# Kernel tuning notes

Measured on AMD Instinct MI355X. Metric: run time of the kernel, lower is better.

The kernel has to match this reference:

```python
import jax, jax.numpy as jnp
import numpy as np

B, C, W, R = 8, 512, 2048, 8
CR = C // R


def setup_inputs() -> dict:
    key = jax.random.key(0)
    ks = jax.random.split(key, 7)
    s = 0.02
    return {
        "x": jax.random.normal(ks[0], (B, C, W), dtype=jnp.float32),
        "wq": jax.random.normal(ks[1], (CR, C), dtype=jnp.float32) * s,
        "bq": jnp.zeros((CR,), dtype=jnp.float32),
        "wk": jax.random.normal(ks[2], (CR, C), dtype=jnp.float32) * s,
        "bk": jnp.zeros((CR,), dtype=jnp.float32),
        "wv": jax.random.normal(ks[3], (C, C), dtype=jnp.float32) * s,
        "bv": jnp.zeros((C,), dtype=jnp.float32),
    }


def reference(x, wq, bq, wk, bk, wv, bv):
    # conv1x1 == per-position linear over channel dim
    q = jnp.einsum("oc,bcw->bow", wq, x) + bq[:, None]   # [B, C//R, W]
    k = jnp.einsum("oc,bcw->bow", wk, x) + bk[:, None]   # [B, C//R, W]
    v = jnp.einsum("oc,bcw->bow", wv, x) + bv[:, None]   # [B, C, W]
    scale = q.shape[1] ** -0.5
    # scores[b, i, j] = sum_d q[b, d, i] * k[b, d, j]
    scores = jnp.einsum("bdi,bdj->bij", q, k) * scale     # [B, W, W]
    attn = jax.nn.softmax(scores, axis=-1)
    # context[b, c, j] = sum_i v[b, c, i] * attn[b, i, j]  (bmm(value, attn))
    context = jnp.einsum("bci,bij->bcj", v, attn)         # [B, C, W]
    return context + x
```

## Files before the change

kernel.cpp:

```cpp
#include <hip/hip_runtime.h>
#include <hip/hip_bf16.h>


#define B 8
#define C 512
#define W 2048
#define CR 64
static constexpr float SCALE = 0.125f;

typedef __bf16 bf16x8 __attribute__((ext_vector_type(8)));
typedef float f32x4 __attribute__((ext_vector_type(4)));
typedef unsigned char uchar;
typedef unsigned long long ull;

__device__ inline ushort f2bs(float f) {
    __hip_bfloat16 h = __float2bfloat16(f);
    return *reinterpret_cast<ushort*>(&h);
}
__device__ inline f32x4 mfma16(bf16x8 a, bf16x8 b, f32x4 c) {
    return __builtin_amdgcn_mfma_f32_16x16x32_bf16(a, b, c, 0, 0, 0);
}
__device__ inline f32x4 mfma8(long long a, long long b, f32x4 c) {
    return __builtin_amdgcn_mfma_f32_16x16x32_fp8_fp8(a, b, c, 0, 0, 0);
}

__device__ inline uchar f2fp8(float f) {
#if __has_builtin(__builtin_amdgcn_cvt_pk_fp8_f32)
    int v = __builtin_amdgcn_cvt_pk_fp8_f32(f, f, 0, false);
    return (uchar)(v & 0xFF);
#else
    unsigned u = __float_as_uint(f);
    uchar s = (uchar)((u >> 24) & 0x80);
    float a = fabsf(f);
    if (a >= 448.0f) return s | 0x7E;
    if (a < 0.015625f) {
        int m = (int)rintf(a * 512.0f);
        if (m > 7) return s | 0x08;
        return s | (uchar)m;
    }
    int e; float m = frexpf(a, &e);
    int Eb = e - 1 + 7;
    int mant = (int)rintf((m * 2.0f - 1.0f) * 8.0f);
    if (mant == 8) { mant = 0; Eb++; }
    if (Eb > 15 || (Eb == 15 && mant > 6)) return s | 0x7E;
    return s | (uchar)(Eb << 3) | (uchar)mant;
#endif
}

__device__ inline size_t vpf8_idx(int b, int c, int i) {
    return (((size_t)(b * 32 + (i >> 6)) * 32 + (c >> 4)) << 10)
         + (((i >> 5) & 1) << 9) + ((((c & 15) | (((i >> 3) & 3) << 4))) << 3) + (i & 7);
}


__global__ __launch_bounds__(256) void cast_w(
    const float* __restrict__ wq, const float* __restrict__ wk, const float* __restrict__ wv,
    ushort* __restrict__ wqb, ushort* __restrict__ wkb, ushort* __restrict__ wvb)
{
    int i = blockIdx.x * 256 + threadIdx.x;
    if (i < CR * C) { wqb[i] = f2bs(wq[i]); wkb[i] = f2bs(wk[i]); }
    if (i < C * C)  { wvb[i] = f2bs(wv[i]); }
}

__global__ __launch_bounds__(256) void castT_kernel(
    const float* __restrict__ x, ushort* __restrict__ xb)
{
    __shared__ __align__(16) ushort tile[64][72];
    const int b = blockIdx.z, c0 = blockIdx.y * 64, w0 = blockIdx.x * 64;
    const int t = threadIdx.x;
    for (int idx = t; idx < 64 * 64; idx += 256) {
        int c = idx >> 6, w = idx & 63;
        tile[w][c] = f2bs(x[(b * C + c0 + c) * W + w0 + w]);
    }
    __syncthreads();
    for (int idx = t; idx < 64 * 8; idx += 256) {
        int w = idx >> 3, u = idx & 7;
        *(bf16x8*)&xb[((size_t)b * W + w0 + w) * C + c0 + u * 8] = *(const bf16x8*)&tile[w][u * 8];
    }
}

__global__ __launch_bounds__(128) void proj_qk2_kernel(
    const ushort* __restrict__ xb, const ushort* __restrict__ wqb, const ushort* __restrict__ wkb,
    const float* __restrict__ bqf, const float* __restrict__ bkf,
    ushort* __restrict__ qT, ushort* __restrict__ kT)
{
    const int bid = blockIdx.x;
    const int b = bid & 7;
    const int w0 = (bid >> 3) * 64 + (threadIdx.x >> 6) * 32;
    const int lane = threadIdx.x & 63;
    const int lr = lane & 15, lg = lane >> 4;

    f32x4 accq[2][4] = {};
    f32x4 acck[2][4] = {};
    for (int kk = 0; kk < 16; ++kk) {
        const int ko = kk * 32 + (lg << 3);
        bf16x8 a[2], fq[4], fk[4];
        #pragma unroll
        for (int mf = 0; mf < 2; ++mf)
            a[mf] = *(const bf16x8*)&xb[((size_t)b * W + w0 + mf * 16 + lr) * C + ko];
        #pragma unroll
        for (int nf = 0; nf < 4; ++nf) {
            fq[nf] = *(const bf16x8*)&wqb[(nf * 16 + lr) * C + ko];
            fk[nf] = *(const bf16x8*)&wkb[(nf * 16 + lr) * C + ko];
        }
        #pragma unroll
        for (int mf = 0; mf < 2; ++mf)
            #pragma unroll
            for (int nf = 0; nf < 4; ++nf) {
                accq[mf][nf] = mfma16(a[mf], fq[nf], accq[mf][nf]);
                acck[mf][nf] = mfma16(a[mf], fk[nf], acck[mf][nf]);
            }
    }
    #pragma unroll
    for (int nf = 0; nf < 4; ++nf) {
        const int d = nf * 16 + lr;
        const float bqv = bqf[d], bkv = bkf[d];
        #pragma unroll
        for (int mf = 0; mf < 2; ++mf)
            #pragma unroll
            for (int r = 0; r < 4; ++r) {
                int w = w0 + mf * 16 + (lg << 2) + r;
                qT[(b * W + w) * CR + d] = f2bs(accq[mf][nf][r] + bqv);
                kT[(b * W + w) * CR + d] = f2bs(acck[mf][nf][r] + bkv);
            }
    }
}

__global__ __launch_bounds__(512) void qk_expf8_kernel(
    const ushort* __restrict__ qT, const ushort* __restrict__ kT,
    uchar* __restrict__ PuF8, float* __restrict__ ilrow)
{
    __shared__ __align__(8) uchar ptb[8][64][72];
    __shared__ float red[8][64];
    const int bid = blockIdx.x;
    const int b = bid & 7;
    const int i0 = (bid >> 3) * 64;
    const int it = i0 >> 6;
    const int t = threadIdx.x;
    const int w = t >> 6, lane = t & 63;
    const int lr = lane & 15, lg = lane >> 4;

    bf16x8 bq[4][2];
    #pragma unroll
    for (int nf = 0; nf < 4; ++nf)
        #pragma unroll
        for (int kk = 0; kk < 2; ++kk)
            bq[nf][kk] = *(const bf16x8*)&qT[(b * W + i0 + nf * 16 + lr) * CR + kk * 32 + (lg << 3)];

    float lacc[4] = {0.f, 0.f, 0.f, 0.f};
    for (int jt = 0; jt < 4; ++jt) {
        const int j0 = (jt * 8 + w) * 64;
        #pragma unroll
        for (int mf = 0; mf < 4; ++mf) {
            bf16x8 akf[2];
            #pragma unroll
            for (int kk = 0; kk < 2; ++kk)
                akf[kk] = *(const bf16x8*)&kT[(b * W + j0 + mf * 16 + lr) * CR + kk * 32 + (lg << 3)];
            f32x4 s[4] = {};
            #pragma unroll
            for (int kk = 0; kk < 2; ++kk)
                #pragma unroll
                for (int nf = 0; nf < 4; ++nf)
                    s[nf] = mfma16(akf[kk], bq[nf][kk], s[nf]);
            #pragma unroll
            for (int nf = 0; nf < 4; ++nf)
                #pragma unroll
                for (int r = 0; r < 4; ++r) {
                    float e = __expf(s[nf][r] * SCALE);
                    lacc[nf] += e;
                    ptb[w][mf * 16 + (lg << 2) + r][nf * 16 + lr] = f2fp8(e);
                }
        }
        #pragma unroll
        for (int mf = 0; mf < 4; ++mf) {
            const int jl = mf * 16 + (lane & 15);
            const size_t tbase = (((size_t)(b * 32 + it) * 128 + (j0 >> 4) + mf) << 10);
            #pragma unroll
            for (int kk = 0; kk < 2; ++kk) {
                const int ikb = (kk << 5) | ((lane >> 4) << 3);
                ull val = *(const ull*)&ptb[w][jl][ikb];
                *(ull*)&PuF8[tbase + (kk << 9) + ((size_t)lane << 3)] = val;
            }
        }
    }
    #pragma unroll
    for (int nf = 0; nf < 4; ++nf) {
        lacc[nf] += __shfl_xor(lacc[nf], 16);
        lacc[nf] += __shfl_xor(lacc[nf], 32);
        if (lg == 0) red[w][nf * 16 + lr] = lacc[nf];
    }
    __syncthreads();
    if (t < 64) {
        float ll = 0.f;
        #pragma unroll
        for (int g = 0; g < 8; ++g) ll += red[g][t];
        ilrow[b * W + i0 + t] = 1.0f / ll;
    }
}

__global__ __launch_bounds__(512) void proj_v2f8_kernel(
    const ushort* __restrict__ xb, const ushort* __restrict__ wvb, const float* __restrict__ bvf,
    const float* __restrict__ ilw, uchar* __restrict__ vpF8)
{
    const int bid = blockIdx.x;
    const int b = bid & 7;
    const int ct = (bid >> 3) & 3;
    const int wt = bid >> 5;
    const int wid = threadIdx.x >> 6, lane = threadIdx.x & 63;
    const int c0 = ct * 128 + (wid >> 2) * 64;
    const int w0 = wt * 256 + (wid & 3) * 64;
    const int lr = lane & 15, lg = lane >> 4;

    f32x4 acc[4][4] = {};
    for (int kk = 0; kk < 16; ++kk) {
        const int ko = kk * 32 + (lg << 3);
        bf16x8 a[4], bb[4];
        #pragma unroll
        for (int mf = 0; mf < 4; ++mf)
            a[mf] = *(const bf16x8*)&wvb[(c0 + mf * 16 + lr) * C + ko];
        #pragma unroll
        for (int nf = 0; nf < 4; ++nf)
            bb[nf] = *(const bf16x8*)&xb[((size_t)b * W + w0 + nf * 16 + lr) * C + ko];
        #pragma unroll
        for (int mf = 0; mf < 4; ++mf)
            #pragma unroll
            for (int nf = 0; nf < 4; ++nf)
                acc[mf][nf] = mfma16(a[mf], bb[nf], acc[mf][nf]);
    }
    float ilv[4];
    #pragma unroll
    for (int nf = 0; nf < 4; ++nf)
        ilv[nf] = ilw[b * W + w0 + nf * 16 + lr] * 1024.0f;
    #pragma unroll
    for (int mf = 0; mf < 4; ++mf) {
        #pragma unroll
        for (int r = 0; r < 4; ++r) {
            const int c = c0 + mf * 16 + (lg << 2) + r;
            const float bvv = bvf[c];
            #pragma unroll
            for (int nf = 0; nf < 4; ++nf) {
                int w = w0 + nf * 16 + lr;
                vpF8[vpf8_idx(b, c, w)] = f2fp8((acc[mf][nf][r] + bvv) * ilv[nf]);
            }
        }
    }
}

__global__ __launch_bounds__(512, 2) void pv38_kernel(
    const float* __restrict__ x, const uchar* __restrict__ vpF8, const uchar* __restrict__ PuF8,
    float* __restrict__ out)
{
    const int bid = blockIdx.x;
    const int b = bid & 7;
    const int j0 = (bid >> 3) * 64;
    const int w = threadIdx.x >> 6, lane = threadIdx.x & 63;
    const int lr = lane & 15, lg = lane >> 4;
    const int c0 = w * 64;
    const int ct0 = c0 >> 4;
    const int jt0 = j0 >> 4;
    const int NIT = W / 64;
    const int lo = lane * 8;

    long long a_cur[4][2], a_nxt[4][2], b_cur[4][2], b_nxt[4][2];
    #pragma unroll
    for (int mf = 0; mf < 4; ++mf)
        #pragma unroll
        for (int kk = 0; kk < 2; ++kk)
            a_cur[mf][kk] = *(const long long*)&vpF8[(((size_t)(b * 32 + 0) * 32 + ct0 + mf) << 10) + (kk << 9) + lo];
    #pragma unroll
    for (int nf = 0; nf < 4; ++nf)
        #pragma unroll
        for (int kk = 0; kk < 2; ++kk)
            b_cur[nf][kk] = *(const long long*)&PuF8[(((size_t)(b * 32 + 0) * 128 + jt0 + nf) << 10) + (kk << 9) + lo];

    f32x4 acc[4][4] = {};
    for (int it = 0; it < NIT; ++it) {
        const int in = (it + 1 < NIT) ? (it + 1) : it;
        #pragma unroll
        for (int mf = 0; mf < 4; ++mf)
            #pragma unroll
            for (int kk = 0; kk < 2; ++kk)
                a_nxt[mf][kk] = *(const long long*)&vpF8[(((size_t)(b * 32 + in) * 32 + ct0 + mf) << 10) + (kk << 9) + lo];
        #pragma unroll
        for (int nf = 0; nf < 4; ++nf)
            #pragma unroll
            for (int kk = 0; kk < 2; ++kk)
                b_nxt[nf][kk] = *(const long long*)&PuF8[(((size_t)(b * 32 + in) * 128 + jt0 + nf) << 10) + (kk << 9) + lo];
        #pragma unroll
        for (int kk = 0; kk < 2; ++kk)
            #pragma unroll
            for (int mf = 0; mf < 4; ++mf)
                #pragma unroll
                for (int nf = 0; nf < 4; ++nf)
                    acc[mf][nf] = mfma8(a_cur[mf][kk], b_cur[nf][kk], acc[mf][nf]);
        #pragma unroll
        for (int mf = 0; mf < 4; ++mf)
            #pragma unroll
            for (int kk = 0; kk < 2; ++kk)
                a_cur[mf][kk] = a_nxt[mf][kk];
        #pragma unroll
        for (int nf = 0; nf < 4; ++nf)
            #pragma unroll
            for (int kk = 0; kk < 2; ++kk)
                b_cur[nf][kk] = b_nxt[nf][kk];
    }
    #pragma unroll
    for (int mf = 0; mf < 4; ++mf)
        #pragma unroll
        for (int nf = 0; nf < 4; ++nf)
            #pragma unroll
            for (int r = 0; r < 4; ++r) {
                int c = c0 + mf * 16 + (lg << 2) + r;
                int j = j0 + nf * 16 + lr;
                int off = (b * C + c) * W + j;
                out[off] = acc[mf][nf][r] * 0.0009765625f + x[off];
            }
}

extern "C" void kernel_launch(void* const* d_in, const int* in_sizes, int n_in,
                              void* d_out, int out_size, void* d_ws, size_t ws_size,
                              hipStream_t stream) {
    const float* x  = (const float*)d_in[0];
    const float* wq = (const float*)d_in[1];
    const float* bq = (const float*)d_in[2];
    const float* wk = (const float*)d_in[3];
    const float* bk = (const float*)d_in[4];
    const float* wv = (const float*)d_in[5];
    const float* bv = (const float*)d_in[6];
    float* out = (float*)d_out;

    char* ws = (char*)d_ws;
    ushort* qTw  = (ushort*)(ws);
    ushort* kTw  = (ushort*)(ws + (2u << 20));
    uchar*  vpF8 = (uchar*)(ws + (4u << 20));
    ushort* xbw  = (ushort*)(ws + (20u << 20));
    ushort* wqb  = (ushort*)(ws + (36u << 20));
    ushort* wkb  = (ushort*)(ws + (36u << 20) + (64u << 10));
    ushort* wvb  = (ushort*)(ws + (36u << 20) + (128u << 10));
    float*  ilrw = (float*)(ws + (36u << 20) + (640u << 10));
    uchar*  PuF8 = (uchar*)(ws + (37u << 20));

    cast_w<<<dim3(1024), 256, 0, stream>>>(wq, wk, wv, wqb, wkb, wvb);
    castT_kernel<<<dim3(W / 64, C / 64, B), 256, 0, stream>>>(x, xbw);
    proj_qk2_kernel<<<dim3(W / 64 * B), 128, 0, stream>>>(xbw, wqb, wkb, bq, bk, qTw, kTw);
    qk_expf8_kernel<<<dim3(W / 64 * B), 512, 0, stream>>>(qTw, kTw, PuF8, ilrw);
    proj_v2f8_kernel<<<dim3(W / 256 * (C / 128) * B), 512, 0, stream>>>(xbw, wvb, bv, ilrw, vpF8);
    pv38_kernel<<<dim3(W / 64 * B), 512, 0, stream>>>(x, vpF8, PuF8, out);
}
```

Before: 127.3 us.

## Split PV kernel K-loop across two wave groups with shared-memory reduction

The PV fp8 GEMM kernel now launches 1024 threads per block. Two halves of 8 waves each process half of the reduction dimension, 16 iterations instead of 32. Their partial accumulators are combined through a shared-memory buffer before the residual add and store. This shortens each wave's serial MFMA/load chain and doubles the waves in flight to hide latency. The cost is extra syncthreads, 32KB of LDS, and possibly fewer resident blocks per CU.

```diff
diff --git a/kernel.cpp b/kernel.cpp
--- a/kernel.cpp
+++ b/kernel.cpp
@@ -246,19 +246,24 @@
     }
 }
 
-__global__ __launch_bounds__(512, 2) void pv38_kernel(
+__global__ __launch_bounds__(1024) void pv38_kernel(
     const float* __restrict__ x, const uchar* __restrict__ vpF8, const uchar* __restrict__ PuF8,
     float* __restrict__ out)
 {
+    __shared__ float redacc[8][64][16];
     const int bid = blockIdx.x;
     const int b = bid & 7;
     const int j0 = (bid >> 3) * 64;
-    const int w = threadIdx.x >> 6, lane = threadIdx.x & 63;
+    const int t = threadIdx.x;
+    const int w16 = t >> 6, lane = t & 63;
+    const int cs = w16 & 7;
+    const int half = w16 >> 3;
     const int lr = lane & 15, lg = lane >> 4;
-    const int c0 = w * 64;
+    const int c0 = cs * 64;
     const int ct0 = c0 >> 4;
     const int jt0 = j0 >> 4;
-    const int NIT = W / 64;
+    const int NIT = 16;
+    const int itb = half * 16;
     const int lo = lane * 8;
 
     long long a_cur[4][2], a_nxt[4][2], b_cur[4][2], b_nxt[4][2];
@@ -266,16 +271,16 @@
     for (int mf = 0; mf < 4; ++mf)
         #pragma unroll
         for (int kk = 0; kk < 2; ++kk)
-            a_cur[mf][kk] = *(const long long*)&vpF8[(((size_t)(b * 32 + 0) * 32 + ct0 + mf) << 10) + (kk << 9) + lo];
+            a_cur[mf][kk] = *(const long long*)&vpF8[(((size_t)(b * 32 + itb) * 32 + ct0 + mf) << 10) + (kk << 9) + lo];
     #pragma unroll
     for (int nf = 0; nf < 4; ++nf)
         #pragma unroll
         for (int kk = 0; kk < 2; ++kk)
-            b_cur[nf][kk] = *(const long long*)&PuF8[(((size_t)(b * 32 + 0) * 128 + jt0 + nf) << 10) + (kk << 9) + lo];
+            b_cur[nf][kk] = *(const long long*)&PuF8[(((size_t)(b * 32 + itb) * 128 + jt0 + nf) << 10) + (kk << 9) + lo];
 
     f32x4 acc[4][4] = {};
     for (int it = 0; it < NIT; ++it) {
-        const int in = (it + 1 < NIT) ? (it + 1) : it;
+        const int in = itb + ((it + 1 < NIT) ? (it + 1) : it);
         #pragma unroll
         for (int mf = 0; mf < 4; ++mf)
             #pragma unroll
@@ -305,16 +310,29 @@
                 b_cur[nf][kk] = b_nxt[nf][kk];
     }
     #pragma unroll
-    for (int mf = 0; mf < 4; ++mf)
-        #pragma unroll
-        for (int nf = 0; nf < 4; ++nf)
-            #pragma unroll
-            for (int r = 0; r < 4; ++r) {
-                int c = c0 + mf * 16 + (lg << 2) + r;
-                int j = j0 + nf * 16 + lr;
-                int off = (b * C + c) * W + j;
-                out[off] = acc[mf][nf][r] * 0.0009765625f + x[off];
-            }
+    for (int mf = 0; mf < 4; ++mf) {
+        __syncthreads();
+        if (half == 1) {
+            #pragma unroll
+            for (int nf = 0; nf < 4; ++nf)
+                #pragma unroll
+                for (int r = 0; r < 4; ++r)
+                    redacc[cs][lane][nf * 4 + r] = acc[mf][nf][r];
+        }
+        __syncthreads();
+        if (half == 0) {
+            #pragma unroll
+            for (int nf = 0; nf < 4; ++nf)
+                #pragma unroll
+                for (int r = 0; r < 4; ++r) {
+                    float sum = acc[mf][nf][r] + redacc[cs][lane][nf * 4 + r];
+                    int c = c0 + mf * 16 + (lg << 2) + r;
+                    int j = j0 + nf * 16 + lr;
+                    int off = (b * C + c) * W + j;
+                    out[off] = sum * 0.0009765625f + x[off];
+                }
+        }
+    }
 }
 
 extern "C" void kernel_launch(void* const* d_in, const int* in_sizes, int n_in,
@@ -345,5 +363,5 @@
     proj_qk2_kernel<<<dim3(W / 64 * B), 128, 0, stream>>>(xbw, wqb, wkb, bq, bk, qTw, kTw);
     qk_expf8_kernel<<<dim3(W / 64 * B), 512, 0, stream>>>(qTw, kTw, PuF8, ilrw);
     proj_v2f8_kernel<<<dim3(W / 256 * (C / 128) * B), 512, 0, stream>>>(xbw, wvb, bv, ilrw, vpF8);
-    pv38_kernel<<<dim3(W / 64 * B), 512, 0, stream>>>(x, vpF8, PuF8, out);
-}
+    pv38_kernel<<<dim3(W / 64 * B), 1024, 0, stream>>>(x, vpF8, PuF8, out);
+}
```

Result: no change. 128.7 us (+1.1%).

## Deepen PV prefetch to two stages and vectorize transpose-cast with larger tiles

Applied to the files above, without the earlier changes.

The PV fp8 MFMA loop now keeps two iterations of A/B fragments in flight instead of one, so global load latency has more time to be hidden behind the MFMAs. The launch-bounds occupancy hint of 2 blocks per CU is dropped so the extra registers fit. The x transpose-cast kernel now uses 128x128 tiles with float4 global loads instead of scalar loads. The risks are lower occupancy in PV from the added registers, and more LDS bank conflicts from the scalar column writes into the padded tile.

```diff
diff --git a/kernel.cpp b/kernel.cpp
--- a/kernel.cpp
+++ b/kernel.cpp
@@ -65,16 +65,21 @@
 __global__ __launch_bounds__(256) void castT_kernel(
     const float* __restrict__ x, ushort* __restrict__ xb)
 {
-    __shared__ __align__(16) ushort tile[64][72];
-    const int b = blockIdx.z, c0 = blockIdx.y * 64, w0 = blockIdx.x * 64;
+    __shared__ __align__(16) ushort tile[128][136];
+    const int b = blockIdx.z, c0 = blockIdx.y * 128, w0 = blockIdx.x * 128;
     const int t = threadIdx.x;
-    for (int idx = t; idx < 64 * 64; idx += 256) {
-        int c = idx >> 6, w = idx & 63;
-        tile[w][c] = f2bs(x[(b * C + c0 + c) * W + w0 + w]);
+    for (int idx = t; idx < 128 * 32; idx += 256) {
+        int c = idx >> 5, u = idx & 31;
+        f32x4 v4 = *(const f32x4*)&x[((size_t)b * C + c0 + c) * W + w0 + u * 4];
+        int w = u * 4;
+        tile[w + 0][c] = f2bs(v4[0]);
+        tile[w + 1][c] = f2bs(v4[1]);
+        tile[w + 2][c] = f2bs(v4[2]);
+        tile[w + 3][c] = f2bs(v4[3]);
     }
     __syncthreads();
-    for (int idx = t; idx < 64 * 8; idx += 256) {
-        int w = idx >> 3, u = idx & 7;
+    for (int idx = t; idx < 128 * 16; idx += 256) {
+        int w = idx >> 4, u = idx & 15;
         *(bf16x8*)&xb[((size_t)b * W + w0 + w) * C + c0 + u * 8] = *(const bf16x8*)&tile[w][u * 8];
     }
 }
@@ -246,7 +251,7 @@
     }
 }
 
-__global__ __launch_bounds__(512, 2) void pv38_kernel(
+__global__ __launch_bounds__(512) void pv38_kernel(
     const float* __restrict__ x, const uchar* __restrict__ vpF8, const uchar* __restrict__ PuF8,
     float* __restrict__ out)
 {
@@ -261,31 +266,36 @@
     const int NIT = W / 64;
     const int lo = lane * 8;
 
-    long long a_cur[4][2], a_nxt[4][2], b_cur[4][2], b_nxt[4][2];
+    long long a_cur[4][2], a_n1[4][2], a_n2[4][2];
+    long long b_cur[4][2], b_n1[4][2], b_n2[4][2];
     #pragma unroll
     for (int mf = 0; mf < 4; ++mf)
         #pragma unroll
-        for (int kk = 0; kk < 2; ++kk)
+        for (int kk = 0; kk < 2; ++kk) {
             a_cur[mf][kk] = *(const long long*)&vpF8[(((size_t)(b * 32 + 0) * 32 + ct0 + mf) << 10) + (kk << 9) + lo];
+            a_n1[mf][kk]  = *(const long long*)&vpF8[(((size_t)(b * 32 + 1) * 32 + ct0 + mf) << 10) + (kk << 9) + lo];
+        }
     #pragma unroll
     for (int nf = 0; nf < 4; ++nf)
         #pragma unroll
-        for (int kk = 0; kk < 2; ++kk)
+        for (int kk = 0; kk < 2; ++kk) {
             b_cur[nf][kk] = *(const long long*)&PuF8[(((size_t)(b * 32 + 0) * 128 + jt0 + nf) << 10) + (kk << 9) + lo];
+            b_n1[nf][kk]  = *(const long long*)&PuF8[(((size_t)(b * 32 + 1) * 128 + jt0 + nf) << 10) + (kk << 9) + lo];
+        }
 
     f32x4 acc[4][4] = {};
     for (int it = 0; it < NIT; ++it) {
-        const int in = (it + 1 < NIT) ? (it + 1) : it;
+        const int in = (it + 2 < NIT) ? (it + 2) : (NIT - 1);
         #pragma unroll
         for (int mf = 0; mf < 4; ++mf)
             #pragma unroll
             for (int kk = 0; kk < 2; ++kk)
-                a_nxt[mf][kk] = *(const long long*)&vpF8[(((size_t)(b * 32 + in) * 32 + ct0 + mf) << 10) + (kk << 9) + lo];
+                a_n2[mf][kk] = *(const long long*)&vpF8[(((size_t)(b * 32 + in) * 32 + ct0 + mf) << 10) + (kk << 9) + lo];
         #pragma unroll
         for (int nf = 0; nf < 4; ++nf)
             #pragma unroll
             for (int kk = 0; kk < 2; ++kk)
-                b_nxt[nf][kk] = *(const long long*)&PuF8[(((size_t)(b * 32 + in) * 128 + jt0 + nf) << 10) + (kk << 9) + lo];
+                b_n2[nf][kk] = *(const long long*)&PuF8[(((size_t)(b * 32 + in) * 128 + jt0 + nf) << 10) + (kk << 9) + lo];
         #pragma unroll
         for (int kk = 0; kk < 2; ++kk)
             #pragma unroll
@@ -296,13 +306,17 @@
         #pragma unroll
         for (int mf = 0; mf < 4; ++mf)
             #pragma unroll
-            for (int kk = 0; kk < 2; ++kk)
-                a_cur[mf][kk] = a_nxt[mf][kk];
+            for (int kk = 0; kk < 2; ++kk) {
+                a_cur[mf][kk] = a_n1[mf][kk];
+                a_n1[mf][kk]  = a_n2[mf][kk];
+            }
         #pragma unroll
         for (int nf = 0; nf < 4; ++nf)
             #pragma unroll
-            for (int kk = 0; kk < 2; ++kk)
-                b_cur[nf][kk] = b_nxt[nf][kk];
+            for (int kk = 0; kk < 2; ++kk) {
+                b_cur[nf][kk] = b_n1[nf][kk];
+                b_n1[nf][kk]  = b_n2[nf][kk];
+            }
     }
     #pragma unroll
     for (int mf = 0; mf < 4; ++mf)
@@ -341,7 +355,7 @@
     uchar*  PuF8 = (uchar*)(ws + (37u << 20));
 
     cast_w<<<dim3(1024), 256, 0, stream>>>(wq, wk, wv, wqb, wkb, wvb);
-    castT_kernel<<<dim3(W / 64, C / 64, B), 256, 0, stream>>>(x, xbw);
+    castT_kernel<<<dim3(W / 128, C / 128, B), 256, 0, stream>>>(x, xbw);
     proj_qk2_kernel<<<dim3(W / 64 * B), 128, 0, stream>>>(xbw, wqb, wkb, bq, bk, qTw, kTw);
     qk_expf8_kernel<<<dim3(W / 64 * B), 512, 0, stream>>>(qTw, kTw, PuF8, ilrw);
     proj_v2f8_kernel<<<dim3(W / 256 * (C / 128) * B), 512, 0, stream>>>(xbw, wvb, bv, ilrw, vpF8);
```

Measured after the change: 143.8 us. +12.9%, slower.

## Fuse weight cast into transpose cast, split QK projection across more waves

Applied to the files above, without the earlier changes.

Folds the separate weight-cast kernel into the x transpose/cast kernel, so each block also converts a slice of wq/wk/wv and one launch goes away. The Q/K projection now runs 512 threads per block, with each wave computing only Q or K for 16 positions instead of both for 32. This gives more waves per block and fewer accumulator registers per wave. The PV kernel also raises wave priority around its MFMA burst. Redundant x-tile loads rise in the projection, and the grid-wide weight-cast indexing relies on enough blocks to cover all weights.

```diff
diff --git a/kernel.cpp b/kernel.cpp
--- a/kernel.cpp
+++ b/kernel.cpp
@@ -52,22 +52,22 @@
          + (((i >> 5) & 1) << 9) + ((((c & 15) | (((i >> 3) & 3) << 4))) << 3) + (i & 7);
 }
 
-
-__global__ __launch_bounds__(256) void cast_w(
+__global__ __launch_bounds__(256) void castTw_kernel(
+    const float* __restrict__ x,
     const float* __restrict__ wq, const float* __restrict__ wk, const float* __restrict__ wv,
+    ushort* __restrict__ xb,
     ushort* __restrict__ wqb, ushort* __restrict__ wkb, ushort* __restrict__ wvb)
-{
-    int i = blockIdx.x * 256 + threadIdx.x;
-    if (i < CR * C) { wqb[i] = f2bs(wq[i]); wkb[i] = f2bs(wk[i]); }
-    if (i < C * C)  { wvb[i] = f2bs(wv[i]); }
-}
-
-__global__ __launch_bounds__(256) void castT_kernel(
-    const float* __restrict__ x, ushort* __restrict__ xb)
 {
     __shared__ __align__(16) ushort tile[64][72];
     const int b = blockIdx.z, c0 = blockIdx.y * 64, w0 = blockIdx.x * 64;
     const int t = threadIdx.x;
+    {
+        const int fb = blockIdx.x + 32 * (blockIdx.y + 8 * blockIdx.z);
+        const int gid = fb * 256 + t;
+        if (gid < CR * C) wqb[gid] = f2bs(wq[gid]);
+        else if (gid < 2 * CR * C) wkb[gid - CR * C] = f2bs(wk[gid - CR * C]);
+        else if (gid < 2 * CR * C + C * C) wvb[gid - 2 * CR * C] = f2bs(wv[gid - 2 * CR * C]);
+    }
     for (int idx = t; idx < 64 * 64; idx += 256) {
         int c = idx >> 6, w = idx & 63;
         tile[w][c] = f2bs(x[(b * C + c0 + c) * W + w0 + w]);
@@ -79,50 +79,43 @@
     }
 }
 
-__global__ __launch_bounds__(128) void proj_qk2_kernel(
+__global__ __launch_bounds__(512) void proj_qk3_kernel(
     const ushort* __restrict__ xb, const ushort* __restrict__ wqb, const ushort* __restrict__ wkb,
     const float* __restrict__ bqf, const float* __restrict__ bkf,
     ushort* __restrict__ qT, ushort* __restrict__ kT)
 {
     const int bid = blockIdx.x;
     const int b = bid & 7;
-    const int w0 = (bid >> 3) * 64 + (threadIdx.x >> 6) * 32;
+    const int isK = (threadIdx.x >> 6) & 1;
+    const int w0 = (bid >> 3) * 64 + (threadIdx.x >> 7) * 16;
     const int lane = threadIdx.x & 63;
     const int lr = lane & 15, lg = lane >> 4;
 
-    f32x4 accq[2][4] = {};
-    f32x4 acck[2][4] = {};
+    const ushort* __restrict__ wb = isK ? wkb : wqb;
+    const float* __restrict__ bb = isK ? bkf : bqf;
+    ushort* __restrict__ outp = isK ? kT : qT;
+
+    f32x4 acc[4] = {};
     for (int kk = 0; kk < 16; ++kk) {
         const int ko = kk * 32 + (lg << 3);
-        bf16x8 a[2], fq[4], fk[4];
-        #pragma unroll
-        for (int mf = 0; mf < 2; ++mf)
-            a[mf] = *(const bf16x8*)&xb[((size_t)b * W + w0 + mf * 16 + lr) * C + ko];
-        #pragma unroll
-        for (int nf = 0; nf < 4; ++nf) {
-            fq[nf] = *(const bf16x8*)&wqb[(nf * 16 + lr) * C + ko];
-            fk[nf] = *(const bf16x8*)&wkb[(nf * 16 + lr) * C + ko];
-        }
-        #pragma unroll
-        for (int mf = 0; mf < 2; ++mf)
-            #pragma unroll
-            for (int nf = 0; nf < 4; ++nf) {
-                accq[mf][nf] = mfma16(a[mf], fq[nf], accq[mf][nf]);
-                acck[mf][nf] = mfma16(a[mf], fk[nf], acck[mf][nf]);
-            }
+        bf16x8 a = *(const bf16x8*)&xb[((size_t)b * W + w0 + lr) * C + ko];
+        bf16x8 fw[4];
+        #pragma unroll
+        for (int nf = 0; nf < 4; ++nf)
+            fw[nf] = *(const bf16x8*)&wb[(nf * 16 + lr) * C + ko];
+        #pragma unroll
+        for (int nf = 0; nf < 4; ++nf)
+            acc[nf] = mfma16(a, fw[nf], acc[nf]);
     }
     #pragma unroll
     for (int nf = 0; nf < 4; ++nf) {
         const int d = nf * 16 + lr;
-        const float bqv = bqf[d], bkv = bkf[d];
-        #pragma unroll
-        for (int mf = 0; mf < 2; ++mf)
-            #pragma unroll
-            for (int r = 0; r < 4; ++r) {
-                int w = w0 + mf * 16 + (lg << 2) + r;
-                qT[(b * W + w) * CR + d] = f2bs(accq[mf][nf][r] + bqv);
-                kT[(b * W + w) * CR + d] = f2bs(acck[mf][nf][r] + bkv);
-            }
+        const float bv = bb[d];
+        #pragma unroll
+        for (int r = 0; r < 4; ++r) {
+            int w = w0 + (lg << 2) + r;
+            outp[(b * W + w) * CR + d] = f2bs(acc[nf][r] + bv);
+        }
     }
 }
 
@@ -214,18 +207,18 @@
     f32x4 acc[4][4] = {};
     for (int kk = 0; kk < 16; ++kk) {
         const int ko = kk * 32 + (lg << 3);
-        bf16x8 a[4], bb[4];
+        bf16x8 a[4], bbv[4];
         #pragma unroll
         for (int mf = 0; mf < 4; ++mf)
             a[mf] = *(const bf16x8*)&wvb[(c0 + mf * 16 + lr) * C + ko];
         #pragma unroll
         for (int nf = 0; nf < 4; ++nf)
-            bb[nf] = *(const bf16x8*)&xb[((size_t)b * W + w0 + nf * 16 + lr) * C + ko];
+            bbv[nf] = *(const bf16x8*)&xb[((size_t)b * W + w0 + nf * 16 + lr) * C + ko];
         #pragma unroll
         for (int mf = 0; mf < 4; ++mf)
             #pragma unroll
             for (int nf = 0; nf < 4; ++nf)
-                acc[mf][nf] = mfma16(a[mf], bb[nf], acc[mf][nf]);
+                acc[mf][nf] = mfma16(a[mf], bbv[nf], acc[mf][nf]);
     }
     float ilv[4];
     #pragma unroll
@@ -286,6 +279,7 @@
             #pragma unroll
             for (int kk = 0; kk < 2; ++kk)
                 b_nxt[nf][kk] = *(const long long*)&PuF8[(((size_t)(b * 32 + in) * 128 + jt0 + nf) << 10) + (kk << 9) + lo];
+        __builtin_amdgcn_s_setprio(1);
         #pragma unroll
         for (int kk = 0; kk < 2; ++kk)
             #pragma unroll
@@ -293,6 +287,7 @@
                 #pragma unroll
                 for (int nf = 0; nf < 4; ++nf)
                     acc[mf][nf] = mfma8(a_cur[mf][kk], b_cur[nf][kk], acc[mf][nf]);
+        __builtin_amdgcn_s_setprio(0);
         #pragma unroll
         for (int mf = 0; mf < 4; ++mf)
             #pragma unroll
@@ -340,9 +335,8 @@
     float*  ilrw = (float*)(ws + (36u << 20) + (640u << 10));
     uchar*  PuF8 = (uchar*)(ws + (37u << 20));
 
-    cast_w<<<dim3(1024), 256, 0, stream>>>(wq, wk, wv, wqb, wkb, wvb);
-    castT_kernel<<<dim3(W / 64, C / 64, B), 256, 0, stream>>>(x, xbw);
-    proj_qk2_kernel<<<dim3(W / 64 * B), 128, 0, stream>>>(xbw, wqb, wkb, bq, bk, qTw, kTw);
+    castTw_kernel<<<dim3(W / 64, C / 64, B), 256, 0, stream>>>(x, wq, wk, wv, xbw, wqb, wkb, wvb);
+    proj_qk3_kernel<<<dim3(W / 64 * B), 512, 0, stream>>>(xbw, wqb, wkb, bq, bk, qTw, kTw);
     qk_expf8_kernel<<<dim3(W / 64 * B), 512, 0, stream>>>(qTw, kTw, PuF8, ilrw);
     proj_v2f8_kernel<<<dim3(W / 256 * (C / 128) * B), 512, 0, stream>>>(xbw, wvb, bv, ilrw, vpF8);
     pv38_kernel<<<dim3(W / 64 * B), 512, 0, stream>>>(x, vpF8, PuF8, out);
```

After: 133.5 us. +4.8%, slower.
